# Performance work log

Hardware: AMD Instinct MI355X
Metric: run time of the kernel (lower is better)

Reference implementation:

```python
import jax, jax.numpy as jnp
import numpy as np
import math


def setup_inputs() -> dict:
    rng = jax.random.key(0)
    k1, k2, k3 = jax.random.split(rng, 3)
    B, L, H, E = 2, 1024, 8, 64
    query = jax.random.normal(k1, (B, L, H, E), dtype=jnp.float32)
    key = jax.random.normal(k2, (B, L, H, E), dtype=jnp.float32)
    value = jax.random.normal(k3, (B, L, H, E), dtype=jnp.float32)
    mask_miss_k = jnp.zeros((B, L), dtype=bool)
    mask_miss_q = jnp.zeros((B, L), dtype=bool)
    pos = jnp.arange(B * L).reshape(B, L)
    causal_mask = 0  # unused by the module body
    # learned scalar parameters (nn.Parameter init values)
    log_gain_gate = jnp.float32(math.log(2.0))
    log_tau_gate = jnp.float32(math.log(0.5))
    log_gain_dir = jnp.float32(math.log(3.0))
    log_tau_dir = jnp.float32(math.log(0.3))
    return {
        "query": query, "key": key, "value": value,
        "mask_miss_k": mask_miss_k, "mask_miss_q": mask_miss_q,
        "pos": pos, "causal_mask": causal_mask,
        "log_gain_gate": log_gain_gate, "log_tau_gate": log_tau_gate,
        "log_gain_dir": log_gain_dir, "log_tau_dir": log_tau_dir,
    }


def reference(query, key, value, mask_miss_k, mask_miss_q, pos, causal_mask,
              log_gain_gate, log_tau_gate, log_gain_dir, log_tau_dir):
    # Multihead path: query (B,L,H,E). Eval mode, dropout p=0, dag_mask=None.
    B, L, H, E = query.shape
    scale = 1.0 / jnp.sqrt(jnp.float32(E))
    # scores: (B,H,L,S) with S == L
    scores = scale * jnp.einsum('blhe,bshe->bhls', query, key)
    scores_t = jnp.swapaxes(scores, -1, -2)
    S_sym = 0.5 * (scores + scores_t)       # symmetric part
    A_anti = 0.5 * (scores - scores_t)      # antisymmetric (Lie) part

    MAX_GAIN = 20.0
    gain_gate = jnp.clip(jnp.exp(log_gain_gate), 1e-3, MAX_GAIN)
    tau_gate = jnp.clip(jnp.exp(log_tau_gate), 1e-3, 10.0)
    gain_dir = jnp.clip(jnp.exp(log_gain_dir), 1e-3, MAX_GAIN)
    tau_dir = jnp.clip(jnp.exp(log_tau_dir), 1e-3, 10.0)

    gamma_att = gain_gate * jnp.tanh(S_sym / tau_gate)
    phi_att = gain_dir * jnp.tanh(A_anti / tau_dir)

    gate_probs = jax.nn.sigmoid(gamma_att)
    dir_probs = jax.nn.sigmoid(phi_att)
    dag_probs = gate_probs * dir_probs

    diag = jnp.eye(L, L, dtype=bool)  # P(i->i) = 0
    dag_probs = jnp.where(diag[None, None], 0.0, dag_probs)
    M = dag_probs  # eval branch; diagonal already zeroed (second fill is a no-op)

    att = jax.nn.relu(jnp.tanh(A_anti * gain_dir / tau_dir)) * M

    # entropy per query position (B,H,L)
    entropy = -jnp.sum(att * jnp.log(jnp.clip(att, 1e-8, None)), axis=-1)
    entropy = jnp.nan_to_num(entropy)

    # dropout p=0 -> identity; nan_to_num is a no-op on finite att
    V = jnp.einsum('bhls,bshd->blhd', att, value)  # (B,L,H,E)
    return V, att, entropy
```

## Files before the change

### kernel.cpp

```cpp
#include <hip/hip_runtime.h>
#include <math.h>

namespace {

typedef __bf16 bf16_t;
typedef bf16_t bf16x8 __attribute__((ext_vector_type(8)));
typedef bf16_t bf16x4 __attribute__((ext_vector_type(4)));
typedef bf16_t bf16x2 __attribute__((ext_vector_type(2)));
typedef float f32x4 __attribute__((ext_vector_type(4)));

constexpr int L = 1024;
constexpr int H = 8;
constexpr int E = 64;
constexpr int HE = H * E;
constexpr int BH = 16;
constexpr size_t PL = (size_t)BH * L * E;
constexpr float LOG2E = 1.4426950408889634f;
constexpr float LN2 = 0.6931471805599453f;

__device__ __forceinline__ float rcp_fast(float x) { return __builtin_amdgcn_rcpf(x); }
__device__ __forceinline__ float exp2_fast(float x) { return __builtin_amdgcn_exp2f(x); }
__device__ __forceinline__ float log2_fast(float x) { return __builtin_amdgcn_logf(x); }
__device__ __forceinline__ f32x4 mfma16(bf16x8 a, bf16x8 b, f32x4 c) {
  return __builtin_amdgcn_mfma_f32_16x16x32_bf16(a, b, c, 0, 0, 0);
}
__device__ __forceinline__ void split4(float4 x, bf16x4& hv, bf16x4& lv) {
  hv[0] = (bf16_t)x.x; lv[0] = (bf16_t)(x.x - (float)hv[0]);
  hv[1] = (bf16_t)x.y; lv[1] = (bf16_t)(x.y - (float)hv[1]);
  hv[2] = (bf16_t)x.z; lv[2] = (bf16_t)(x.z - (float)hv[2]);
  hv[3] = (bf16_t)x.w; lv[3] = (bf16_t)(x.w - (float)hv[3]);
}

__global__ __launch_bounds__(256) void k_prep(
    const float* __restrict__ q, const float* __restrict__ k,
    const float* __restrict__ v, bf16_t* __restrict__ ws,
    float* __restrict__ Vout, float* __restrict__ entr)
{
  const int bid = blockIdx.x;
  if (bid >= 256) {
    const int idx = (bid - 256) * 256 + threadIdx.x;
    const float4 z = make_float4(0.f, 0.f, 0.f, 0.f);
    if (idx < 262144) *(float4*)(Vout + (size_t)idx * 4) = z;
    else              *(float4*)(entr + (size_t)(idx - 262144) * 4) = z;
    return;
  }
  bf16_t* Qh = ws;
  bf16_t* Ql = ws + PL;
  bf16_t* Kh = ws + 2 * PL;
  bf16_t* Kl = ws + 3 * PL;
  bf16_t* VT = ws + 4 * PL;
  const int bh = bid >> 4, chunk = bid & 15;
  const int b = bh >> 3, h = bh & 7;
  const int tid = threadIdx.x, t8 = tid >> 4, c4 = tid & 15;
  __shared__ bf16_t Vb[64][72];

#pragma unroll
  for (int pass = 0; pass < 4; ++pass) {
    const int row = chunk * 64 + pass * 16 + t8;
    const size_t gin = ((size_t)(b * L + row) * H + h) * E + c4 * 4;
    const size_t gout = ((size_t)bh * L + row) * E + c4 * 4;
    float4 q4 = *(const float4*)(q + gin);
    float4 k4 = *(const float4*)(k + gin);
    float4 v4 = *(const float4*)(v + gin);
    bf16x4 hv, lv;
    split4(q4, hv, lv);
    *(bf16x4*)(Qh + gout) = hv; *(bf16x4*)(Ql + gout) = lv;
    split4(k4, hv, lv);
    *(bf16x4*)(Kh + gout) = hv; *(bf16x4*)(Kl + gout) = lv;
    const int sl = pass * 16 + t8;
    Vb[c4 * 4 + 0][sl] = (bf16_t)v4.x;
    Vb[c4 * 4 + 1][sl] = (bf16_t)v4.y;
    Vb[c4 * 4 + 2][sl] = (bf16_t)v4.z;
    Vb[c4 * 4 + 3][sl] = (bf16_t)v4.w;
  }
  __syncthreads();
#pragma unroll
  for (int pass = 0; pass < 2; ++pass) {
    const int idx = pass * 256 + tid;
    const int e = idx >> 3, ch = idx & 7;
    bf16x8 val = *(const bf16x8*)&Vb[e][ch * 8];
    *(bf16x8*)(VT + ((size_t)bh * E + e) * L + chunk * 64 + ch * 8) = val;
  }
}

__global__ __launch_bounds__(256, 3) void k_main(
    const bf16_t* __restrict__ ws,
    float* __restrict__ Vout, float* __restrict__ attg, float* __restrict__ entr,
    const float* __restrict__ p_lgg, const float* __restrict__ p_ltg,
    const float* __restrict__ p_lgd, const float* __restrict__ p_ltd)
{
  const bf16_t* Qh = ws;
  const bf16_t* Ql = ws + PL;
  const bf16_t* Kh = ws + 2 * PL;
  const bf16_t* Kl = ws + 3 * PL;
  const bf16_t* VT = ws + 4 * PL;

  __shared__ __align__(16) char smem[32768];
  bf16_t (*KQh)[72]  = (bf16_t(*)[72])(smem);
  bf16_t (*KQl)[72]  = (bf16_t(*)[72])(smem + 9216);
  bf16_t (*Vt)[72]   = (bf16_t(*)[72])(smem + 18432);
  bf16_t (*attL)[40] = (bf16_t(*)[40])(smem + 27648);

  const int tid = threadIdx.x;
  const int w = tid >> 6, lane = tid & 63;
  const int c = lane & 15, qd = lane >> 4;
  const int lh = w & 1, sh = w >> 1;
  const int lt = blockIdx.x, bh = blockIdx.y, zb = blockIdx.z;
  const int b = bh >> 3, h = bh & 7;
  const int l0 = lt * 32;

  const float gg = fminf(fmaxf(__expf(p_lgg[0]), 1e-3f), 20.0f);
  const float tg = fminf(fmaxf(__expf(p_ltg[0]), 1e-3f), 10.0f);
  const float gd = fminf(fmaxf(__expf(p_lgd[0]), 1e-3f), 20.0f);
  const float td = fminf(fmaxf(__expf(p_ltd[0]), 1e-3f), 10.0f);
  const float A1 = 0.125f * (1.0f / tg) * LOG2E;
  const float A2 = 0.125f * (1.0f / td) * LOG2E;
  const float A3 = 0.125f * gd * (1.0f / td) * LOG2E;
  const float G1 = -gg * LOG2E;
  const float G2 = -gd * LOG2E;

  bf16x8 qaf[2][2], kaf[2][2];
  {
    const size_t aro = ((size_t)bh * L + l0 + lh * 16 + c) * E;
#pragma unroll
    for (int ks = 0; ks < 2; ++ks) {
      qaf[ks][0] = *(const bf16x8*)(Qh + aro + ks * 32 + qd * 8);
      qaf[ks][1] = *(const bf16x8*)(Ql + aro + ks * 32 + qd * 8);
      kaf[ks][0] = *(const bf16x8*)(Kh + aro + ks * 32 + qd * 8);
      kaf[ks][1] = *(const bf16x8*)(Kl + aro + ks * 32 + qd * 8);
    }
  }

  const int srow = tid >> 2, scol = (tid & 3) * 16;

  bf16x8 kh8a, kh8b, kl8a, kl8b, vt8a, vt8b, qh8a, qh8b, ql8a, ql8b;
  {
    const int s0 = zb * 4 * 64;
    const size_t off = ((size_t)bh * L + s0 + srow) * E + scol;
    kh8a = *(const bf16x8*)(Kh + off);
    kh8b = *(const bf16x8*)(Kh + off + 8);
    kl8a = *(const bf16x8*)(Kl + off);
    kl8b = *(const bf16x8*)(Kl + off + 8);
    const size_t voff = ((size_t)bh * E + srow) * L + s0 + scol;
    vt8a = *(const bf16x8*)(VT + voff);
    vt8b = *(const bf16x8*)(VT + voff + 8);
  }

  f32x4 accv[4] = {};
  float ent[4] = {0.f, 0.f, 0.f, 0.f};

  for (int it = 0; it < 4; ++it) {
    const int ti = zb * 4 + it;
    const int s0 = ti * 64;
    const int s0n = ((ti + 1) & 15) * 64;

    __syncthreads();
    *(bf16x8*)&KQh[srow][scol]     = kh8a;
    *(bf16x8*)&KQh[srow][scol + 8] = kh8b;
    *(bf16x8*)&KQl[srow][scol]     = kl8a;
    *(bf16x8*)&KQl[srow][scol + 8] = kl8b;
    *(bf16x8*)&Vt[srow][scol]      = vt8a;
    *(bf16x8*)&Vt[srow][scol + 8]  = vt8b;
    {
      const size_t off = ((size_t)bh * L + s0 + srow) * E + scol;
      qh8a = *(const bf16x8*)(Qh + off);
      qh8b = *(const bf16x8*)(Qh + off + 8);
      ql8a = *(const bf16x8*)(Ql + off);
      ql8b = *(const bf16x8*)(Ql + off + 8);
    }
    __syncthreads();

    f32x4 acc1[2] = {}, acc2[2] = {};
#pragma unroll
    for (int nt = 0; nt < 2; ++nt) {
      const int brow = sh * 32 + nt * 16 + c;
#pragma unroll
      for (int ks = 0; ks < 2; ++ks) {
        bf16x8 bhv = *(const bf16x8*)&KQh[brow][ks * 32 + qd * 8];
        bf16x8 blv = *(const bf16x8*)&KQl[brow][ks * 32 + qd * 8];
        acc1[nt] = mfma16(qaf[ks][0], bhv, acc1[nt]);
        acc1[nt] = mfma16(qaf[ks][0], blv, acc1[nt]);
        acc1[nt] = mfma16(qaf[ks][1], bhv, acc1[nt]);
      }
    }
    __syncthreads();

    *(bf16x8*)&KQh[srow][scol]     = qh8a;
    *(bf16x8*)&KQh[srow][scol + 8] = qh8b;
    *(bf16x8*)&KQl[srow][scol]     = ql8a;
    *(bf16x8*)&KQl[srow][scol + 8] = ql8b;
    {
      const size_t off = ((size_t)bh * L + s0n + srow) * E + scol;
      kh8a = *(const bf16x8*)(Kh + off);
      kh8b = *(const bf16x8*)(Kh + off + 8);
      kl8a = *(const bf16x8*)(Kl + off);
      kl8b = *(const bf16x8*)(Kl + off + 8);
      const size_t voff = ((size_t)bh * E + srow) * L + s0n + scol;
      vt8a = *(const bf16x8*)(VT + voff);
      vt8b = *(const bf16x8*)(VT + voff + 8);
    }
    __syncthreads();

#pragma unroll
    for (int nt = 0; nt < 2; ++nt) {
      const int brow = sh * 32 + nt * 16 + c;
#pragma unroll
      for (int ks = 0; ks < 2; ++ks) {
        bf16x8 qbh = *(const bf16x8*)&KQh[brow][ks * 32 + qd * 8];
        bf16x8 qbl = *(const bf16x8*)&KQl[brow][ks * 32 + qd * 8];
        acc2[nt] = mfma16(kaf[ks][0], qbh, acc2[nt]);
        acc2[nt] = mfma16(kaf[ks][1], qbh, acc2[nt]);
        acc2[nt] = mfma16(kaf[ks][0], qbl, acc2[nt]);
      }
    }

    float* arow = attg + ((size_t)bh * L + l0 + lh * 16 + qd * 4) * L + s0 + sh * 32;
#pragma unroll
    for (int nt = 0; nt < 2; ++nt) {
#pragma unroll
      for (int r = 0; r < 4; ++r) {
        float u = acc1[nt][r] + acc2[nt][r];
        float d = acc1[nt][r] - acc2[nt][r];
        float th1 = 1.f - 2.f * rcp_fast(exp2_fast(u * A1) + 1.f);
        float gate = rcp_fast(1.f + exp2_fast(th1 * G1));
        float th2 = 1.f - 2.f * rcp_fast(exp2_fast(d * A2) + 1.f);
        float dir  = rcp_fast(1.f + exp2_fast(th2 * G2));
        float t    = 1.f - 2.f * rcp_fast(exp2_fast(d * A3) + 1.f);
        float a = fmaxf(t, 0.0f) * gate * dir;
        ent[r] -= a * log2_fast(fmaxf(a, 1e-8f));
        arow[(size_t)r * L + nt * 16 + c] = a;
        attL[w * 16 + qd * 4 + r][nt * 16 + c] = (bf16_t)a;
      }
    }
    __threadfence_block();

    bf16x8 af = *(const bf16x8*)&attL[w * 16 + c][qd * 8];
#pragma unroll
    for (int ne = 0; ne < 4; ++ne) {
      bf16x8 bv = *(const bf16x8*)&Vt[ne * 16 + c][sh * 32 + qd * 8];
      accv[ne] = mfma16(af, bv, accv[ne]);
    }
  }

  __syncthreads();
  float* red = (float*)smem;
  if (sh == 1) {
#pragma unroll
    for (int ne = 0; ne < 4; ++ne)
#pragma unroll
      for (int r = 0; r < 4; ++r)
        red[((size_t)lh * 16 + qd * 4 + r) * 68 + ne * 16 + c] = accv[ne][r];
  }
  __syncthreads();
  if (sh == 0) {
#pragma unroll
    for (int ne = 0; ne < 4; ++ne)
#pragma unroll
      for (int r = 0; r < 4; ++r) {
        float val = accv[ne][r] +
                    red[((size_t)lh * 16 + qd * 4 + r) * 68 + ne * 16 + c];
        atomicAdd(Vout + ((size_t)(b * L + l0 + lh * 16 + qd * 4 + r) * H + h) * E +
                      ne * 16 + c,
                  val);
      }
  }
#pragma unroll
  for (int r = 0; r < 4; ++r) {
    float e = ent[r];
    e += __shfl_xor(e, 1);
    e += __shfl_xor(e, 2);
    e += __shfl_xor(e, 4);
    e += __shfl_xor(e, 8);
    if (c == 0)
      atomicAdd(entr + (size_t)bh * L + l0 + lh * 16 + qd * 4 + r, e * LN2);
  }
}

__device__ __forceinline__ float tanh_fast(float x) {
  return 1.0f - 2.0f * rcp_fast(__expf(2.0f * x) + 1.0f);
}
__device__ __forceinline__ float sigm_fast(float x) {
  return rcp_fast(1.0f + __expf(-x));
}
__device__ __forceinline__ void split_store(bf16_t* hi, bf16_t* lo, float4 x) {
  bf16x4 hv, lv;
  split4(x, hv, lv);
  *(bf16x4*)hi = hv;
  *(bf16x4*)lo = lv;
}

__global__ __launch_bounds__(128, 1) void fused_attn(
    const float* __restrict__ q, const float* __restrict__ kk,
    const float* __restrict__ v,
    float* __restrict__ Vout, float* __restrict__ attg, float* __restrict__ entr,
    const float* __restrict__ p_lgg, const float* __restrict__ p_ltg,
    const float* __restrict__ p_lgd, const float* __restrict__ p_ltd)
{
  constexpr int TM = 32;
  __shared__ bf16_t Qa_hi[TM][72], Qa_lo[TM][72];
  __shared__ bf16_t Ka_hi[TM][72], Ka_lo[TM][72];
  __shared__ bf16_t KQ_hi[64][72], KQ_lo[64][72];
  __shared__ bf16_t Vts[64][72];
  __shared__ float  T2ex[2][64][17];
  __shared__ bf16_t attLs[2][16][72];

  const int tid = threadIdx.x;
  const int w = tid >> 6;
  const int lane = tid & 63;
  const int c = lane & 15;
  const int qd = lane >> 4;
  const int t8 = tid >> 4;
  const int c4 = tid & 15;
  const int lt = blockIdx.x;
  const int bh = blockIdx.y;
  const int b = bh >> 3, h = bh & 7;
  const int l0 = lt * TM;

  const float gg = fminf(fmaxf(__expf(p_lgg[0]), 1e-3f), 20.0f);
  const float tg = fminf(fmaxf(__expf(p_ltg[0]), 1e-3f), 10.0f);
  const float gd = fminf(fmaxf(__expf(p_lgd[0]), 1e-3f), 20.0f);
  const float td = fminf(fmaxf(__expf(p_ltd[0]), 1e-3f), 10.0f);
  const float inv_tg = 1.0f / tg;
  const float inv_td = 1.0f / td;
  const float gd_inv_td = gd * inv_td;

  const float* qlbase = q  + ((size_t)(b * L + l0) * H + h) * E;
  const float* qsbase = q  + ((size_t)b * L * H + h) * E;
  const float* kbase  = kk + ((size_t)b * L * H + h) * E;
  const float* vbase  = v  + ((size_t)b * L * H + h) * E;

#pragma unroll
  for (int i = 0; i < 4; ++i) {
    int r = t8 + 8 * i;
    float4 qa = *(const float4*)(qlbase + (size_t)r * HE + c4 * 4);
    float4 ka = *(const float4*)(kbase + (size_t)(l0 + r) * HE + c4 * 4);
    split_store(&Qa_hi[r][c4 * 4], &Qa_lo[r][c4 * 4], qa);
    split_store(&Ka_hi[r][c4 * 4], &Ka_lo[r][c4 * 4], ka);
  }

  float4 kpre[8], qpre[8];
  float vpre[32];
#pragma unroll
  for (int i = 0; i < 8; ++i)
    kpre[i] = *(const float4*)(kbase + (size_t)(t8 + 8 * i) * HE + c4 * 4);
#pragma unroll
  for (int i = 0; i < 8; ++i)
    qpre[i] = *(const float4*)(qsbase + (size_t)(t8 + 8 * i) * HE + c4 * 4);
#pragma unroll
  for (int j = 0; j < 32; ++j)
    vpre[j] = vbase[(size_t)(w * 32 + j) * HE + lane];

  __syncthreads();

  bf16x8 qaf[2][2], kaf[2][2];
#pragma unroll
  for (int ks = 0; ks < 2; ++ks) {
    qaf[ks][0] = *(const bf16x8*)&Qa_hi[w * 16 + c][ks * 32 + qd * 8];
    qaf[ks][1] = *(const bf16x8*)&Qa_lo[w * 16 + c][ks * 32 + qd * 8];
    kaf[ks][0] = *(const bf16x8*)&Ka_hi[w * 16 + c][ks * 32 + qd * 8];
    kaf[ks][1] = *(const bf16x8*)&Ka_lo[w * 16 + c][ks * 32 + qd * 8];
  }

  f32x4 accv[4] = {};
  float ent[4] = {0.f, 0.f, 0.f, 0.f};
  const int gl_base = l0 + w * 16 + qd * 4;

  for (int it = 0; it < 16; ++it) {
    const int s0 = it * 64;
    const int snext = ((it + 1) & 15) * 64;

    __syncthreads();
#pragma unroll
    for (int i = 0; i < 8; ++i) {
      int r = t8 + 8 * i;
      split_store(&KQ_hi[r][c4 * 4], &KQ_lo[r][c4 * 4], kpre[i]);
    }
#pragma unroll
    for (int j = 0; j < 16; ++j) {
      bf16x2 p;
      p[0] = (bf16_t)vpre[2 * j];
      p[1] = (bf16_t)vpre[2 * j + 1];
      *(bf16x2*)&Vts[lane][w * 32 + 2 * j] = p;
    }
    __syncthreads();

#pragma unroll
    for (int i = 0; i < 8; ++i)
      kpre[i] = *(const float4*)(kbase + (size_t)(snext + t8 + 8 * i) * HE + c4 * 4);
#pragma unroll
    for (int j = 0; j < 32; ++j)
      vpre[j] = vbase[(size_t)(snext + w * 32 + j) * HE + lane];

    f32x4 acc1[4] = {};
#pragma unroll
    for (int nt = 0; nt < 4; ++nt) {
#pragma unroll
      for (int ks = 0; ks < 2; ++ks) {
        bf16x8 bhv = *(const bf16x8*)&KQ_hi[nt * 16 + c][ks * 32 + qd * 8];
        bf16x8 blv = *(const bf16x8*)&KQ_lo[nt * 16 + c][ks * 32 + qd * 8];
        acc1[nt] = mfma16(qaf[ks][0], bhv, acc1[nt]);
        acc1[nt] = mfma16(qaf[ks][0], blv, acc1[nt]);
        acc1[nt] = mfma16(qaf[ks][1], bhv, acc1[nt]);
      }
    }
    __syncthreads();

#pragma unroll
    for (int i = 0; i < 8; ++i) {
      int r = t8 + 8 * i;
      split_store(&KQ_hi[r][c4 * 4], &KQ_lo[r][c4 * 4], qpre[i]);
    }
    __syncthreads();

#pragma unroll
    for (int i = 0; i < 8; ++i)
      qpre[i] = *(const float4*)(qsbase + (size_t)(snext + t8 + 8 * i) * HE + c4 * 4);

    f32x4 acc2[4] = {};
#pragma unroll
    for (int mt = 0; mt < 4; ++mt) {
#pragma unroll
      for (int ks = 0; ks < 2; ++ks) {
        bf16x8 ahv = *(const bf16x8*)&KQ_hi[mt * 16 + c][ks * 32 + qd * 8];
        bf16x8 alv = *(const bf16x8*)&KQ_lo[mt * 16 + c][ks * 32 + qd * 8];
        acc2[mt] = mfma16(ahv, kaf[ks][0], acc2[mt]);
        acc2[mt] = mfma16(ahv, kaf[ks][1], acc2[mt]);
        acc2[mt] = mfma16(alv, kaf[ks][0], acc2[mt]);
      }
    }

#pragma unroll
    for (int mt = 0; mt < 4; ++mt)
#pragma unroll
      for (int r = 0; r < 4; ++r)
        T2ex[w][mt * 16 + qd * 4 + r][c] = acc2[mt][r];
    __syncthreads();

    float* attrow0 = attg + ((size_t)bh * L + gl_base) * L + s0;
#pragma unroll
    for (int nt = 0; nt < 4; ++nt) {
#pragma unroll
      for (int r = 0; r < 4; ++r) {
        float x = 0.125f * acc1[nt][r];
        float y = 0.125f * T2ex[w][nt * 16 + c][qd * 4 + r];
        float Ss = 0.5f * (x + y);
        float Aa = 0.5f * (x - y);
        float gate = sigm_fast(gg * tanh_fast(Ss * inv_tg));
        float dir  = sigm_fast(gd * tanh_fast(Aa * inv_td));
        float t    = tanh_fast(Aa * gd_inv_td);
        float a = fmaxf(t, 0.0f) * gate * dir;
        ent[r] -= a * __logf(fmaxf(a, 1e-8f));
        attrow0[(size_t)r * L + nt * 16 + c] = a;
        attLs[w][qd * 4 + r][nt * 16 + c] = (bf16_t)a;
      }
    }
    __syncthreads();

#pragma unroll
    for (int ks = 0; ks < 2; ++ks) {
      bf16x8 af = *(const bf16x8*)&attLs[w][c][ks * 32 + qd * 8];
#pragma unroll
      for (int ne = 0; ne < 4; ++ne) {
        bf16x8 bfv = *(const bf16x8*)&Vts[ne * 16 + c][ks * 32 + qd * 8];
        accv[ne] = mfma16(af, bfv, accv[ne]);
      }
    }
  }

#pragma unroll
  for (int r = 0; r < 4; ++r) {
    float* vb = Vout + ((size_t)(b * L + gl_base + r) * H + h) * E;
#pragma unroll
    for (int ne = 0; ne < 4; ++ne) vb[ne * 16 + c] = accv[ne][r];
    float e4 = ent[r];
    e4 += __shfl_xor(e4, 1);
    e4 += __shfl_xor(e4, 2);
    e4 += __shfl_xor(e4, 4);
    e4 += __shfl_xor(e4, 8);
    if (c == 0) entr[(size_t)bh * L + gl_base + r] = e4;
  }
}

}

extern "C" void kernel_launch(void* const* d_in, const int* in_sizes, int n_in,
                              void* d_out, int out_size, void* d_ws, size_t ws_size,
                              hipStream_t stream) {
  const float* q = (const float*)d_in[0];
  const float* k = (const float*)d_in[1];
  const float* v = (const float*)d_in[2];
  const float* p_lgg = (const float*)d_in[7];
  const float* p_ltg = (const float*)d_in[8];
  const float* p_lgd = (const float*)d_in[9];
  const float* p_ltd = (const float*)d_in[10];

  float* Vout = (float*)d_out;
  float* att  = Vout + 1048576;
  float* entr = att + 16777216;

  const size_t need = 5 * PL * sizeof(bf16_t);
  if (ws_size >= need) {
    bf16_t* ws = (bf16_t*)d_ws;
    k_prep<<<dim3(1296), 256, 0, stream>>>(q, k, v, ws, Vout, entr);
    k_main<<<dim3(32, 16, 4), 256, 0, stream>>>(
        ws, Vout, att, entr, p_lgg, p_ltg, p_lgd, p_ltd);
  } else {
    fused_attn<<<dim3(32, 16), 128, 0, stream>>>(
        q, k, v, Vout, att, entr, p_lgg, p_ltg, p_lgd, p_ltd);
  }
}
```

Measured before the change: 137.8 us.

## Load MFMA B-operands directly from global memory, dropping LDS staging and barriers

Removes the shared-memory staging of K, Q and V^T tiles, along with the four __syncthreads per iteration. Each wave now loads its MFMA B fragments straight from global memory into registers and fully unrolls the loop. The attention output is written with nontemporal stores. This drops LDS traffic and block barriers, but each wave issues more scattered global loads that rely on L1/L2 reuse, and register pressure rises.

```diff
diff --git a/kernel.cpp b/kernel.cpp
--- a/kernel.cpp
+++ b/kernel.cpp
@@ -95,11 +95,8 @@
   const bf16_t* Kl = ws + 3 * PL;
   const bf16_t* VT = ws + 4 * PL;
 
-  __shared__ __align__(16) char smem[32768];
-  bf16_t (*KQh)[72]  = (bf16_t(*)[72])(smem);
-  bf16_t (*KQl)[72]  = (bf16_t(*)[72])(smem + 9216);
-  bf16_t (*Vt)[72]   = (bf16_t(*)[72])(smem + 18432);
-  bf16_t (*attL)[40] = (bf16_t(*)[40])(smem + 27648);
+  __shared__ bf16_t attL[4][16][40];
+  __shared__ float red[32][68];
 
   const int tid = threadIdx.x;
   const int w = tid >> 6, lane = tid & 63;
@@ -131,86 +128,43 @@
     }
   }
 
-  const int srow = tid >> 2, scol = (tid & 3) * 16;
-
-  bf16x8 kh8a, kh8b, kl8a, kl8b, vt8a, vt8b, qh8a, qh8b, ql8a, ql8b;
-  {
-    const int s0 = zb * 4 * 64;
-    const size_t off = ((size_t)bh * L + s0 + srow) * E + scol;
-    kh8a = *(const bf16x8*)(Kh + off);
-    kh8b = *(const bf16x8*)(Kh + off + 8);
-    kl8a = *(const bf16x8*)(Kl + off);
-    kl8b = *(const bf16x8*)(Kl + off + 8);
-    const size_t voff = ((size_t)bh * E + srow) * L + s0 + scol;
-    vt8a = *(const bf16x8*)(VT + voff);
-    vt8b = *(const bf16x8*)(VT + voff + 8);
-  }
-
   f32x4 accv[4] = {};
   float ent[4] = {0.f, 0.f, 0.f, 0.f};
 
+#pragma unroll
   for (int it = 0; it < 4; ++it) {
-    const int ti = zb * 4 + it;
-    const int s0 = ti * 64;
-    const int s0n = ((ti + 1) & 15) * 64;
-
-    __syncthreads();
-    *(bf16x8*)&KQh[srow][scol]     = kh8a;
-    *(bf16x8*)&KQh[srow][scol + 8] = kh8b;
-    *(bf16x8*)&KQl[srow][scol]     = kl8a;
-    *(bf16x8*)&KQl[srow][scol + 8] = kl8b;
-    *(bf16x8*)&Vt[srow][scol]      = vt8a;
-    *(bf16x8*)&Vt[srow][scol + 8]  = vt8b;
-    {
-      const size_t off = ((size_t)bh * L + s0 + srow) * E + scol;
-      qh8a = *(const bf16x8*)(Qh + off);
-      qh8b = *(const bf16x8*)(Qh + off + 8);
-      ql8a = *(const bf16x8*)(Ql + off);
-      ql8b = *(const bf16x8*)(Ql + off + 8);
-    }
-    __syncthreads();
+    const int s0 = (zb * 4 + it) * 64;
+
+    bf16x8 kbh[2][2], kbl[2][2], qbh[2][2], qbl[2][2];
+    const size_t bro = ((size_t)bh * L + s0 + sh * 32 + c) * E + qd * 8;
+#pragma unroll
+    for (int nt = 0; nt < 2; ++nt) {
+#pragma unroll
+      for (int ks = 0; ks < 2; ++ks) {
+        const size_t o = bro + (size_t)nt * 16 * E + ks * 32;
+        kbh[nt][ks] = *(const bf16x8*)(Kh + o);
+        kbl[nt][ks] = *(const bf16x8*)(Kl + o);
+        qbh[nt][ks] = *(const bf16x8*)(Qh + o);
+        qbl[nt][ks] = *(const bf16x8*)(Ql + o);
+      }
+    }
+    bf16x8 vbv[4];
+#pragma unroll
+    for (int ne = 0; ne < 4; ++ne)
+      vbv[ne] = *(const bf16x8*)(VT + ((size_t)bh * E + ne * 16 + c) * L +
+                                 s0 + sh * 32 + qd * 8);
 
     f32x4 acc1[2] = {}, acc2[2] = {};
 #pragma unroll
     for (int nt = 0; nt < 2; ++nt) {
-      const int brow = sh * 32 + nt * 16 + c;
 #pragma unroll
       for (int ks = 0; ks < 2; ++ks) {
-        bf16x8 bhv = *(const bf16x8*)&KQh[brow][ks * 32 + qd * 8];
-        bf16x8 blv = *(const bf16x8*)&KQl[brow][ks * 32 + qd * 8];
-        acc1[nt] = mfma16(qaf[ks][0], bhv, acc1[nt]);
-        acc1[nt] = mfma16(qaf[ks][0], blv, acc1[nt]);
-        acc1[nt] = mfma16(qaf[ks][1], bhv, acc1[nt]);
-      }
-    }
-    __syncthreads();
-
-    *(bf16x8*)&KQh[srow][scol]     = qh8a;
-    *(bf16x8*)&KQh[srow][scol + 8] = qh8b;
-    *(bf16x8*)&KQl[srow][scol]     = ql8a;
-    *(bf16x8*)&KQl[srow][scol + 8] = ql8b;
-    {
-      const size_t off = ((size_t)bh * L + s0n + srow) * E + scol;
-      kh8a = *(const bf16x8*)(Kh + off);
-      kh8b = *(const bf16x8*)(Kh + off + 8);
-      kl8a = *(const bf16x8*)(Kl + off);
-      kl8b = *(const bf16x8*)(Kl + off + 8);
-      const size_t voff = ((size_t)bh * E + srow) * L + s0n + scol;
-      vt8a = *(const bf16x8*)(VT + voff);
-      vt8b = *(const bf16x8*)(VT + voff + 8);
-    }
-    __syncthreads();
-
-#pragma unroll
-    for (int nt = 0; nt < 2; ++nt) {
-      const int brow = sh * 32 + nt * 16 + c;
-#pragma unroll
-      for (int ks = 0; ks < 2; ++ks) {
-        bf16x8 qbh = *(const bf16x8*)&KQh[brow][ks * 32 + qd * 8];
-        bf16x8 qbl = *(const bf16x8*)&KQl[brow][ks * 32 + qd * 8];
-        acc2[nt] = mfma16(kaf[ks][0], qbh, acc2[nt]);
-        acc2[nt] = mfma16(kaf[ks][1], qbh, acc2[nt]);
-        acc2[nt] = mfma16(kaf[ks][0], qbl, acc2[nt]);
+        acc1[nt] = mfma16(qaf[ks][0], kbh[nt][ks], acc1[nt]);
+        acc1[nt] = mfma16(qaf[ks][0], kbl[nt][ks], acc1[nt]);
+        acc1[nt] = mfma16(qaf[ks][1], kbh[nt][ks], acc1[nt]);
+        acc2[nt] = mfma16(kaf[ks][0], qbh[nt][ks], acc2[nt]);
+        acc2[nt] = mfma16(kaf[ks][1], qbh[nt][ks], acc2[nt]);
+        acc2[nt] = mfma16(kaf[ks][0], qbl[nt][ks], acc2[nt]);
       }
     }
 
@@ -228,28 +182,24 @@
         float t    = 1.f - 2.f * rcp_fast(exp2_fast(d * A3) + 1.f);
         float a = fmaxf(t, 0.0f) * gate * dir;
         ent[r] -= a * log2_fast(fmaxf(a, 1e-8f));
-        arow[(size_t)r * L + nt * 16 + c] = a;
-        attL[w * 16 + qd * 4 + r][nt * 16 + c] = (bf16_t)a;
+        __builtin_nontemporal_store(a, arow + (size_t)r * L + nt * 16 + c);
+        attL[w][qd * 4 + r][nt * 16 + c] = (bf16_t)a;
       }
     }
     __threadfence_block();
 
-    bf16x8 af = *(const bf16x8*)&attL[w * 16 + c][qd * 8];
-#pragma unroll
-    for (int ne = 0; ne < 4; ++ne) {
-      bf16x8 bv = *(const bf16x8*)&Vt[ne * 16 + c][sh * 32 + qd * 8];
-      accv[ne] = mfma16(af, bv, accv[ne]);
-    }
-  }
-
-  __syncthreads();
-  float* red = (float*)smem;
+    bf16x8 af = *(const bf16x8*)&attL[w][c][qd * 8];
+#pragma unroll
+    for (int ne = 0; ne < 4; ++ne)
+      accv[ne] = mfma16(af, vbv[ne], accv[ne]);
+  }
+
   if (sh == 1) {
 #pragma unroll
     for (int ne = 0; ne < 4; ++ne)
 #pragma unroll
       for (int r = 0; r < 4; ++r)
-        red[((size_t)lh * 16 + qd * 4 + r) * 68 + ne * 16 + c] = accv[ne][r];
+        red[lh * 16 + qd * 4 + r][ne * 16 + c] = accv[ne][r];
   }
   __syncthreads();
   if (sh == 0) {
@@ -257,8 +207,7 @@
     for (int ne = 0; ne < 4; ++ne)
 #pragma unroll
       for (int r = 0; r < 4; ++r) {
-        float val = accv[ne][r] +
-                    red[((size_t)lh * 16 + qd * 4 + r) * 68 + ne * 16 + c];
+        float val = accv[ne][r] + red[lh * 16 + qd * 4 + r][ne * 16 + c];
         atomicAdd(Vout + ((size_t)(b * L + l0 + lh * 16 + qd * 4 + r) * H + h) * E +
                       ne * 16 + c,
                   val);
```

After: 183.0 us. 1.33x slower.
